# Kernel optimization log

Measured on AMD Instinct MI355X. Metric: run time of the kernel, lower is better.

Reference implementation:

```python
import jax, jax.numpy as jnp
import numpy as np

F = 128; K = 64; SR_CUT = 10.0
NB = 5; NRI = 3; NRA = 2; NRO = 1
N_ATOMS = 10000; N_PAIRS = 320000


def act(x):
    # shifted softplus: softplus(x) - log(2)
    return jax.nn.softplus(x) - jnp.log(2.0).astype(x.dtype)


def residual(x, W1, b1, W2, b2):
    # PhysNet residual: x + dense2(dense1(act(x))) with activation on dense1
    h = act(act(x) @ W1 + b1)
    return x + h @ W2 + b2


def cutoff_fn(D):
    x = D / SR_CUT
    x3 = x * x * x; x4 = x3 * x; x5 = x4 * x
    return jnp.where(x < 1.0, 1.0 - 6.0 * x5 + 15.0 * x4 - 10.0 * x3, 0.0)


def setup_inputs() -> dict:
    key = jax.random.key(0)
    ks = jax.random.split(key, 24)

    def nrm(k, shape, s=0.05):
        return (jax.random.normal(k, shape) * s).astype(jnp.float32)

    inp = {}
    inp["Z"] = jax.random.randint(ks[0], (N_ATOMS,), 1, 95)
    inp["R"] = (jax.random.normal(ks[1], (N_ATOMS, 3)) * 3.0).astype(jnp.float32)
    inp["idx_i"] = jax.random.randint(ks[2], (N_PAIRS,), 0, N_ATOMS)
    inp["idx_j"] = jax.random.randint(ks[3], (N_PAIRS,), 0, N_ATOMS)
    s3 = float(np.sqrt(3.0))
    inp["embeddings"] = jax.random.uniform(ks[4], (95, F), minval=-s3, maxval=s3).astype(jnp.float32)
    inp["rbf_centers"] = jnp.linspace(1.0, float(np.exp(-SR_CUT)), K).astype(jnp.float32)
    width = (0.5 / ((1.0 - float(np.exp(-SR_CUT))) / K)) ** 2
    inp["rbf_widths"] = jnp.full((K,), width, dtype=jnp.float32)
    inp["k2f_W"] = nrm(ks[5], (NB, K, F))
    inp["Wi"] = nrm(ks[6], (NB, F, F)); inp["bi"] = jnp.zeros((NB, F), jnp.float32)
    inp["Wj"] = nrm(ks[7], (NB, F, F)); inp["bj"] = jnp.zeros((NB, F), jnp.float32)
    inp["ri_W1"] = nrm(ks[8], (NB, NRI, F, F)); inp["ri_b1"] = jnp.zeros((NB, NRI, F), jnp.float32)
    inp["ri_W2"] = nrm(ks[9], (NB, NRI, F, F)); inp["ri_b2"] = jnp.zeros((NB, NRI, F), jnp.float32)
    inp["dW"] = nrm(ks[10], (NB, F, F)); inp["db"] = jnp.zeros((NB, F), jnp.float32)
    inp["u"] = jnp.ones((NB, F), jnp.float32)
    inp["ra_W1"] = nrm(ks[11], (NB, NRA, F, F)); inp["ra_b1"] = jnp.zeros((NB, NRA, F), jnp.float32)
    inp["ra_W2"] = nrm(ks[12], (NB, NRA, F, F)); inp["ra_b2"] = jnp.zeros((NB, NRA, F), jnp.float32)
    inp["ro_W1"] = nrm(ks[13], (NB, NRO, F, F)); inp["ro_b1"] = jnp.zeros((NB, NRO, F), jnp.float32)
    inp["ro_W2"] = nrm(ks[14], (NB, NRO, F, F)); inp["ro_b2"] = jnp.zeros((NB, NRO, F), jnp.float32)
    inp["out_W"] = nrm(ks[15], (NB, F, 2))
    inp["Escale"] = jnp.ones((95,), jnp.float32); inp["Eshift"] = jnp.zeros((95,), jnp.float32)
    inp["Qscale"] = jnp.ones((95,), jnp.float32); inp["Qshift"] = jnp.zeros((95,), jnp.float32)
    return inp


def reference(Z, R, idx_i, idx_j, embeddings, rbf_centers, rbf_widths, k2f_W, Wi, bi, Wj, bj,
              ri_W1, ri_b1, ri_W2, ri_b2, dW, db, u, ra_W1, ra_b1, ra_W2, ra_b2,
              ro_W1, ro_b1, ro_W2, ro_b2, out_W, Escale, Eshift, Qscale, Qshift):
    N = R.shape[0]
    # gather-based interatomic distances: gather -> sub -> sumsq -> relu -> sqrt
    dR = R[idx_i] - R[idx_j]                                   # [P,3]
    Dij = jnp.sqrt(jax.nn.relu(jnp.sum(dR * dR, axis=-1)))     # [P]
    # RBF expansion with smooth cutoff
    rbf = cutoff_fn(Dij)[:, None] * jnp.exp(-rbf_widths * (jnp.exp(-Dij)[:, None] - rbf_centers) ** 2)  # [P,K]
    x = embeddings[Z]                                          # [N,F]
    Ea = jnp.zeros((N,), x.dtype)
    Qa = jnp.zeros((N,), x.dtype)
    nhloss = jnp.zeros((), x.dtype)
    last2 = None
    for b in range(NB):
        # --- interaction layer ---
        g = rbf @ k2f_W[b]                                     # [P,F]
        xa = act(x)
        xi = act(xa @ Wi[b] + bi[b])                           # [N,F]
        xj_feat = act(xa @ Wj[b] + bj[b])                      # [N,F]
        msg = g * xj_feat[idx_j]                               # [P,F] gather + modulate
        m = xi + jax.ops.segment_sum(msg, idx_i, num_segments=N)
        for l in range(NRI):
            m = residual(m, ri_W1[b, l], ri_b1[b, l], ri_W2[b, l], ri_b2[b, l])
        m = act(m)
        x = u[b] * x + m @ dW[b] + db[b]
        for l in range(NRA):
            x = residual(x, ra_W1[b, l], ra_b1[b, l], ra_W2[b, l], ra_b2[b, l])
        # --- output block ---
        o = x
        for l in range(NRO):
            o = residual(o, ro_W1[b, l], ro_b1[b, l], ro_W2[b, l], ro_b2[b, l])
        out = act(o) @ out_W[b]                                # [N,2] -> (Ea, Qa)
        Ea = Ea + out[:, 0]
        Qa = Qa + out[:, 1]
        out2 = out * out
        if b > 0:
            nhloss = nhloss + jnp.mean(out2 / (out2 + last2 + 1e-7))
        last2 = out2
    Ea = Escale[Z] * Ea + Eshift[Z]
    Qa = Qscale[Z] * Qa + Qshift[Z]
    return Ea, Qa, Dij, nhloss
```

## Files before the change

kernel.cpp:

```cpp
#include <hip/hip_runtime.h>

typedef __attribute__((ext_vector_type(8))) short bfrag;
typedef __attribute__((ext_vector_type(4))) float ffrag;

__device__ __forceinline__ unsigned short f2b(float f){
  unsigned int u = __float_as_uint(f);
  return (unsigned short)((u + 0x7FFFu + ((u >> 16) & 1u)) >> 16);
}
__device__ __forceinline__ float b2f_lo(unsigned int v){
  return __uint_as_float(v << 16);
}
__device__ __forceinline__ float b2f_hi(unsigned int v){
  return __uint_as_float(v & 0xFFFF0000u);
}
__device__ __forceinline__ int rfl(int v){ return __builtin_amdgcn_readfirstlane(v); }
__device__ __forceinline__ float actf(float v){
  float e = __builtin_amdgcn_exp2f(-fabsf(v)*1.44269504088896341f);
  return fmaxf(v, 0.f) + __builtin_amdgcn_logf(1.f + e)*0.69314718055994531f - 0.69314718055994531f;
}

__global__ __launch_bounds__(256) void k_zero(float* p, int n){
  int i = blockIdx.x*256 + threadIdx.x;
  if (i < n) p[i] = 0.f;
}

__global__ __launch_bounds__(256) void k_dij_count(
    const float* __restrict__ R, const int* __restrict__ idx_i, const int* __restrict__ idx_j,
    float* __restrict__ DijF, float* __restrict__ Dout, int* __restrict__ counts, int P){
  int p = blockIdx.x*256 + threadIdx.x;
  if (p >= P) return;
  int i = idx_i[p], j = idx_j[p];
  float dx = R[i*3+0] - R[j*3+0];
  float dy = R[i*3+1] - R[j*3+1];
  float dz = R[i*3+2] - R[j*3+2];
  float D = sqrtf(fmaxf(dx*dx + dy*dy + dz*dz, 0.f));
  DijF[p] = D;
  Dout[p] = D;
  atomicAdd(&counts[i], 1);
}

__global__ __launch_bounds__(1024) void k_scan(const int* __restrict__ counts,
    int* __restrict__ cursor, int N){
  __shared__ int wsum[16];
  int tid = threadIdx.x;
  int CH = (N + 1023) >> 10;
  int base = tid * CH;
  int s = 0;
  for (int i = 0; i < CH; ++i){
    int idx = base + i;
    s += (idx < N) ? counts[idx] : 0;
  }
  int lane = tid & 63, w = tid >> 6;
  int v = s;
  #pragma unroll
  for (int off = 1; off < 64; off <<= 1){
    int t = __shfl_up(v, off, 64);
    if (lane >= off) v += t;
  }
  if (lane == 63) wsum[w] = v;
  __syncthreads();
  if (tid < 16){
    int t = wsum[tid];
    int vv = t;
    #pragma unroll
    for (int off = 1; off < 16; off <<= 1){
      int u = __shfl_up(vv, off, 64);
      if (tid >= off) vv += u;
    }
    wsum[tid] = vv - t;
  }
  __syncthreads();
  int run = (v - s) + wsum[w];
  for (int i = 0; i < CH; ++i){
    int idx = base + i;
    if (idx < N){ cursor[idx] = run; run += counts[idx]; }
  }
}

__global__ __launch_bounds__(256) void k_scatter(const int* __restrict__ idx_i,
    const int* __restrict__ idx_j, const float* __restrict__ DijF,
    int* __restrict__ cursor, int* __restrict__ i_s, int* __restrict__ j_s,
    float* __restrict__ D_s, int P){
  int p = blockIdx.x*256 + threadIdx.x;
  if (p >= P) return;
  int i = idx_i[p];
  int pos = atomicAdd(&cursor[i], 1);
  i_s[pos] = i;
  j_s[pos] = idx_j[p];
  D_s[pos] = DijF[p];
}

__global__ __launch_bounds__(256) void k_prep2(
    const float* __restrict__ D_s, const float* __restrict__ cent, const float* __restrict__ wid,
    unsigned short* __restrict__ rbf_s,
    const float* __restrict__ riW1, const float* __restrict__ riW2,
    const float* __restrict__ dW,   const float* __restrict__ raW1,
    const float* __restrict__ raW2, const float* __restrict__ roW1,
    const float* __restrict__ roW2, const float* __restrict__ Wi,
    const float* __restrict__ Wj,   const float* __restrict__ k2f,
    const float* __restrict__ outW,
    unsigned short* __restrict__ WBall, unsigned short* __restrict__ k2fP,
    unsigned short* __restrict__ outWB, int P){
  int gid0 = blockIdx.x*256 + threadIdx.x;
  if (gid0 < P*8){
    int t = gid0 >> 3, kg = gid0 & 7;
    float D = D_s[t];
    float xc = D * 0.1f;
    float cut = 0.f;
    if (xc < 1.f){
      float x3 = xc*xc*xc, x4 = x3*xc, x5 = x4*xc;
      cut = 1.f - 6.f*x5 + 15.f*x4 - 10.f*x3;
    }
    float eD = __builtin_amdgcn_exp2f(-D*1.44269504088896341f);
    bfrag o;
    #pragma unroll
    for (int i = 0; i < 8; ++i){
      int k = kg*8 + i;
      float tt = eD - cent[k];
      float v = cut * __builtin_amdgcn_exp2f(-wid[k]*tt*tt*1.44269504088896341f);
      o[i] = (short)f2b(v);
    }
    *(bfrag*)(rbf_s + (size_t)gid0*8) = o;
    return;
  }
  int gid = gid0 - P*8;
  if (gid < 75*2048){
    int i = gid >> 11, r = gid & 2047;
    const float* S;
    int slot;
    if (i < 15)      { S = riW1 + (size_t)i*16384;      slot = (i/3)*15 + 2*(i%3); }
    else if (i < 30) { int j=i-15; S = riW2 + (size_t)j*16384; slot = (j/3)*15 + 2*(j%3) + 1; }
    else if (i < 35) { int j=i-30; S = dW   + (size_t)j*16384; slot = j*15 + 6; }
    else if (i < 45) { int j=i-35; S = raW1 + (size_t)j*16384; slot = (j/2)*15 + 7 + 2*(j%2); }
    else if (i < 55) { int j=i-45; S = raW2 + (size_t)j*16384; slot = (j/2)*15 + 8 + 2*(j%2); }
    else if (i < 60) { int j=i-55; S = roW1 + (size_t)j*16384; slot = j*15 + 11; }
    else if (i < 65) { int j=i-60; S = roW2 + (size_t)j*16384; slot = j*15 + 12; }
    else if (i < 70) { int j=i-65; S = Wi   + (size_t)j*16384; slot = ((j==0)?4:(j-1))*15 + 13; }
    else             { int j=i-70; S = Wj   + (size_t)j*16384; slot = ((j==0)?4:(j-1))*15 + 14; }
    int fr = r >> 6, l = r & 63;
    int T = fr >> 2, k0 = fr & 3;
    int n = T*16 + (l & 15);
    int kbase = k0*32 + (l >> 4)*8;
    unsigned short* D = WBall + ((size_t)slot*2048 + r)*8;
    ushort4 o0, o1;
    o0.x=f2b(S[(kbase+0)*128+n]); o0.y=f2b(S[(kbase+1)*128+n]);
    o0.z=f2b(S[(kbase+2)*128+n]); o0.w=f2b(S[(kbase+3)*128+n]);
    o1.x=f2b(S[(kbase+4)*128+n]); o1.y=f2b(S[(kbase+5)*128+n]);
    o1.z=f2b(S[(kbase+6)*128+n]); o1.w=f2b(S[(kbase+7)*128+n]);
    ((ushort4*)D)[0]=o0; ((ushort4*)D)[1]=o1;
  } else if (gid < 75*2048 + 5120){
    int g = gid - 75*2048;
    int l = g & 63, fr = (g >> 6) & 15, b = g >> 10;
    int tile = fr >> 1, kh = fr & 1;
    const float* src = k2f + (size_t)b*64*128;
    int n = tile*16 + (l & 15);
    int kbase = kh*32 + (l >> 4)*8;
    ushort4 o0, o1;
    o0.x = f2b(src[(kbase+0)*128+n]); o0.y = f2b(src[(kbase+1)*128+n]);
    o0.z = f2b(src[(kbase+2)*128+n]); o0.w = f2b(src[(kbase+3)*128+n]);
    o1.x = f2b(src[(kbase+4)*128+n]); o1.y = f2b(src[(kbase+5)*128+n]);
    o1.z = f2b(src[(kbase+6)*128+n]); o1.w = f2b(src[(kbase+7)*128+n]);
    ushort4* dst = (ushort4*)(k2fP + (size_t)g*8);
    dst[0] = o0; dst[1] = o1;
  } else if (gid < 75*2048 + 5120 + 1280){
    int g = gid - (75*2048 + 5120);
    int b = g >> 8, r = g & 255;
    int l = r & 63;
    int col = l & 15;
    int k0 = r >> 6;
    int kbase = k0*32 + (l >> 4)*8;
    ushort4 o0 = {0,0,0,0}, o1 = {0,0,0,0};
    if (col < 2){
      const float* S = outW + (size_t)b*256;
      o0.x=f2b(S[(kbase+0)*2+col]); o0.y=f2b(S[(kbase+1)*2+col]);
      o0.z=f2b(S[(kbase+2)*2+col]); o0.w=f2b(S[(kbase+3)*2+col]);
      o1.x=f2b(S[(kbase+4)*2+col]); o1.y=f2b(S[(kbase+5)*2+col]);
      o1.z=f2b(S[(kbase+6)*2+col]); o1.w=f2b(S[(kbase+7)*2+col]);
    }
    unsigned short* D = outWB + ((size_t)b*256 + r)*8;
    ((ushort4*)D)[0]=o0; ((ushort4*)D)[1]=o1;
  }
}

__device__ __forceinline__ void mmtile(const unsigned short* tile,
    const unsigned short* __restrict__ WB, int w, int l, ffrag C[4]){
  int m = l & 15, q = l >> 4;
  bfrag A[4];
  #pragma unroll
  for (int k0 = 0; k0 < 4; ++k0)
    A[k0] = *(const bfrag*)(tile + m*136 + k0*32 + q*8);
  #pragma unroll
  for (int tt = 0; tt < 4; ++tt){
    ffrag c = {0.f,0.f,0.f,0.f};
    const bfrag* bp = (const bfrag*)(WB + (((w*4+tt)*4)*64 + l)*8);
    #pragma unroll
    for (int k0 = 0; k0 < 4; ++k0)
      c = __builtin_amdgcn_mfma_f32_16x16x32_bf16(A[k0], bp[k0*64], c, 0, 0, 0);
    C[tt] = c;
  }
}

__global__ __launch_bounds__(128) void k_phase1m(
    const int* __restrict__ Z, const float* __restrict__ emb,
    const unsigned short* __restrict__ WB45,
    const float* __restrict__ bi0, const float* __restrict__ bj0,
    float* __restrict__ x_g, float* __restrict__ m_g, unsigned short* __restrict__ xjb_g, int N){
  __shared__ unsigned short tile[16*136];
  int tid = threadIdx.x, w = tid >> 6, l = tid & 63;
  int m = l & 15, q = l >> 4, rbase = blockIdx.x*16;
  #pragma unroll
  for (int r = 0; r < 4; ++r){
    int row = rbase + q*4 + r;
    int z = Z[row];
    #pragma unroll
    for (int tt = 0; tt < 4; ++tt){
      int c = (w*4+tt)*16 + m;
      float v = emb[(size_t)z*128 + c];
      x_g[(size_t)row*128 + c] = v;
      tile[(q*4+r)*136 + c] = f2b(actf(v));
    }
  }
  __syncthreads();
  ffrag C[4];
  mmtile(tile, WB45 + 13*16384, w, l, C);
  #pragma unroll
  for (int tt = 0; tt < 4; ++tt){
    int c = (w*4+tt)*16 + m;
    float bb = bi0[c];
    #pragma unroll
    for (int r = 0; r < 4; ++r)
      m_g[(size_t)(rbase + q*4 + r)*128 + c] = actf(C[tt][r] + bb);
  }
  mmtile(tile, WB45 + 14*16384, w, l, C);
  #pragma unroll
  for (int tt = 0; tt < 4; ++tt){
    int c = (w*4+tt)*16 + m;
    float bb = bj0[c];
    #pragma unroll
    for (int r = 0; r < 4; ++r)
      xjb_g[(size_t)(rbase + q*4 + r)*128 + c] = f2b(actf(C[tt][r] + bb));
  }
}

__global__ __launch_bounds__(256, 4) void k_pairmsg2(
    const unsigned short* __restrict__ rbf_s, const unsigned short* __restrict__ k2fP,
    const int* __restrict__ i_s, const int* __restrict__ j_s,
    const unsigned short* __restrict__ xj, float* __restrict__ m_g, int P){
  __shared__ float G[4][16*130];
  int tid = threadIdx.x, w = tid >> 6, l = tid & 63;
  float* Gw = &G[w][0];
  bfrag B[16];
  #pragma unroll
  for (int t = 0; t < 16; ++t)
    B[t] = *(const bfrag*)(k2fP + (size_t)(t*64 + l)*8);
  int wstart = (blockIdx.x*4 + w)*64;
  if (wstart >= P) return;
  int row16 = l & 15, quad = l >> 4;
  float a0 = 0.f, a1 = 0.f;
  int iCur = -1;
  #pragma unroll 1
  for (int bi2 = 0; bi2 < 4; ++bi2){
    int bt = wstart + bi2*16;
    bfrag A0 = *(const bfrag*)(rbf_s + (size_t)(bt + row16)*64 + quad*8);
    bfrag A1 = *(const bfrag*)(rbf_s + (size_t)(bt + row16)*64 + 32 + quad*8);
    int ip[16], jp[16];
    #pragma unroll
    for (int g = 0; g < 4; ++g){
      int4 it = *(const int4*)(i_s + bt + g*4);
      int4 jt = *(const int4*)(j_s + bt + g*4);
      ip[g*4+0]=rfl(it.x); ip[g*4+1]=rfl(it.y); ip[g*4+2]=rfl(it.z); ip[g*4+3]=rfl(it.w);
      jp[g*4+0]=rfl(jt.x); jp[g*4+1]=rfl(jt.y); jp[g*4+2]=rfl(jt.z); jp[g*4+3]=rfl(jt.w);
    }
    unsigned int xv[16];
    #pragma unroll
    for (int k = 0; k < 16; ++k)
      xv[k] = *(const unsigned int*)(xj + (size_t)jp[k]*128 + 2*l);
    #pragma unroll
    for (int t = 0; t < 8; ++t){
      ffrag C = {0.f,0.f,0.f,0.f};
      C = __builtin_amdgcn_mfma_f32_16x16x32_bf16(A0, B[t*2],   C, 0, 0, 0);
      C = __builtin_amdgcn_mfma_f32_16x16x32_bf16(A1, B[t*2+1], C, 0, 0, 0);
      #pragma unroll
      for (int r = 0; r < 4; ++r)
        Gw[(quad*4+r)*130 + t*16 + row16] = C[r];
    }
    #pragma unroll
    for (int k = 0; k < 16; ++k){
      int i = ip[k];
      if (i != iCur){
        if (iCur >= 0){
          unsafeAtomicAdd(&m_g[(size_t)iCur*128 + 2*l],     a0);
          unsafeAtomicAdd(&m_g[(size_t)iCur*128 + 2*l + 1], a1);
        }
        iCur = i; a0 = 0.f; a1 = 0.f;
      }
      float g0 = Gw[k*130 + 2*l], g1 = Gw[k*130 + 2*l + 1];
      a0 = fmaf(g0, b2f_lo(xv[k]), a0);
      a1 = fmaf(g1, b2f_hi(xv[k]), a1);
    }
  }
  if (iCur >= 0){
    unsafeAtomicAdd(&m_g[(size_t)iCur*128 + 2*l],     a0);
    unsafeAtomicAdd(&m_g[(size_t)iCur*128 + 2*l + 1], a1);
  }
}

template<int HASNEXT, int NH>
__global__ __launch_bounds__(512) void k_phase2m(
    float* __restrict__ m_g, float* __restrict__ x_g, unsigned short* __restrict__ xjb_g,
    const unsigned short* __restrict__ WBb,
    const float* __restrict__ rib1, const float* __restrict__ rib2,
    const float* __restrict__ db, const float* __restrict__ u,
    const float* __restrict__ rab1, const float* __restrict__ rab2,
    const float* __restrict__ rob1, const float* __restrict__ rob2,
    const float* __restrict__ biN, const float* __restrict__ bjN,
    const unsigned short* __restrict__ outWBb,
    float* __restrict__ Ea, float* __restrict__ Qa,
    float* __restrict__ last2, float* __restrict__ nh, int N){
  __shared__ unsigned short tiles[2][2][16*136];
  __shared__ float biasS[16*128];
  int tid = threadIdx.x, w = tid >> 6, l = tid & 63;
  int m = l & 15, q = l >> 4, rbase = blockIdx.x*32;
  int c = w*16 + m;
  ffrag mC[2], xC[2], C[2];
  float xrow[2][4];
  int cur = 0;
  const int nst = HASNEXT ? 15 : 13;
  const int slotSeq[15] = {0,1,2,3,4,5,6,7,8,9,10,
                           HASNEXT?13:11, HASNEXT?14:12, 11, 12};
  bfrag Bb[2][4];
  #pragma unroll
  for (int k0 = 0; k0 < 4; ++k0)
    Bb[0][k0] = *(const bfrag*)(WBb + (size_t)slotSeq[0]*16384 + (size_t)((w*4+k0)*64 + l)*8);

  if (tid < 128){
    biasS[0*128+tid]  = rib1[tid];
    biasS[1*128+tid]  = rib1[128+tid];
    biasS[2*128+tid]  = rib1[256+tid];
    biasS[3*128+tid]  = rib2[tid];
    biasS[4*128+tid]  = rib2[128+tid];
    biasS[5*128+tid]  = rib2[256+tid];
    biasS[6*128+tid]  = db[tid];
    biasS[7*128+tid]  = u[tid];
    biasS[8*128+tid]  = rab1[tid];
    biasS[9*128+tid]  = rab1[128+tid];
    biasS[10*128+tid] = rab2[tid];
    biasS[11*128+tid] = rab2[128+tid];
    biasS[12*128+tid] = rob1[tid];
    biasS[13*128+tid] = rob2[tid];
    biasS[14*128+tid] = biN[tid];
    biasS[15*128+tid] = bjN[tid];
  }
  #pragma unroll
  for (int h = 0; h < 2; ++h){
    #pragma unroll
    for (int r = 0; r < 4; ++r){
      int row = rbase + h*16 + q*4 + r;
      int rs = row < N ? row : N-1;
      xrow[h][r] = x_g[(size_t)rs*128 + c];
      float v = m_g[(size_t)rs*128 + c];
      mC[h][r] = v;
      tiles[h][0][(q*4+r)*136 + c] = f2b(actf(v));
    }
  }
  #pragma unroll 2
  for (int s = 0; s < nst; ++s){
    __syncthreads();
    if (s+1 < nst){
      #pragma unroll
      for (int k0 = 0; k0 < 4; ++k0)
        Bb[(s+1)&1][k0] = *(const bfrag*)(WBb + (size_t)slotSeq[s+1]*16384 + (size_t)((w*4+k0)*64 + l)*8);
    }
    #pragma unroll
    for (int h = 0; h < 2; ++h){
      const unsigned short* tp = &tiles[h][cur][0];
      ffrag cc = {0.f,0.f,0.f,0.f};
      #pragma unroll
      for (int k0 = 0; k0 < 4; ++k0){
        bfrag A = *(const bfrag*)(tp + m*136 + k0*32 + q*8);
        cc = __builtin_amdgcn_mfma_f32_16x16x32_bf16(A, Bb[s&1][k0], cc, 0, 0, 0);
      }
      C[h] = cc;
    }
    if (HASNEXT && s == 11){
      float bb = biasS[14*128 + c];
      #pragma unroll
      for (int h = 0; h < 2; ++h)
        #pragma unroll
        for (int r = 0; r < 4; ++r){
          int row = rbase + h*16 + q*4 + r;
          if (row < N) m_g[(size_t)row*128 + c] = actf(C[h][r] + bb);
        }
    } else if (HASNEXT && s == 12){
      float bb = biasS[15*128 + c];
      #pragma unroll
      for (int h = 0; h < 2; ++h)
        #pragma unroll
        for (int r = 0; r < 4; ++r){
          int row = rbase + h*16 + q*4 + r;
          if (row < N) xjb_g[(size_t)row*128 + c] = f2b(actf(C[h][r] + bb));
        }
    } else if (s == 6){
      float uu = biasS[7*128 + c], bb = biasS[6*128 + c];
      #pragma unroll
      for (int h = 0; h < 2; ++h)
        #pragma unroll
        for (int r = 0; r < 4; ++r){
          float nv = uu*xrow[h][r] + C[h][r] + bb;
          xC[h][r] = nv;
          tiles[h][1-cur][(q*4+r)*136 + c] = f2b(actf(nv));
        }
      cur ^= 1;
    } else if (s == 1 || s == 3 || s == 5){
      float bb = biasS[(3 + (s>>1))*128 + c];
      #pragma unroll
      for (int h = 0; h < 2; ++h)
        #pragma unroll
        for (int r = 0; r < 4; ++r){
          float nv = mC[h][r] + C[h][r] + bb;
          mC[h][r] = nv;
          tiles[h][1-cur][(q*4+r)*136 + c] = f2b(actf(nv));
        }
      cur ^= 1;
    } else if (s == 8 || s == 10){
      float bb = biasS[(10 + ((s-8)>>1))*128 + c];
      #pragma unroll
      for (int h = 0; h < 2; ++h)
        #pragma unroll
        for (int r = 0; r < 4; ++r){
          float nv = xC[h][r] + C[h][r] + bb;
          xC[h][r] = nv;
          tiles[h][1-cur][(q*4+r)*136 + c] = f2b(actf(nv));
          if (HASNEXT && s == 10){
            int row = rbase + h*16 + q*4 + r;
            if (row < N) x_g[(size_t)row*128 + c] = nv;
          }
        }
      cur ^= 1;
    } else if ((HASNEXT && s == 14) || (!HASNEXT && s == 12)){
      float bb = biasS[13*128 + c];
      #pragma unroll
      for (int h = 0; h < 2; ++h)
        #pragma unroll
        for (int r = 0; r < 4; ++r){
          float ov = xC[h][r] + C[h][r] + bb;
          tiles[h][1-cur][(q*4+r)*136 + c] = f2b(actf(ov));
        }
      cur ^= 1;
    } else {
      int bidx = (s==0)?0:(s==2)?1:(s==4)?2:(s==7)?8:(s==9)?9:12;
      float bb = biasS[bidx*128 + c];
      #pragma unroll
      for (int h = 0; h < 2; ++h)
        #pragma unroll
        for (int r = 0; r < 4; ++r)
          tiles[h][1-cur][(q*4+r)*136 + c] = f2b(actf(C[h][r] + bb));
      cur ^= 1;
    }
  }
  __syncthreads();
  if (w < 2){
    const unsigned short* tp = &tiles[w][cur][0];
    bfrag A[4];
    #pragma unroll
    for (int k0 = 0; k0 < 4; ++k0)
      A[k0] = *(const bfrag*)(tp + m*136 + k0*32 + q*8);
    ffrag Ch = {0.f,0.f,0.f,0.f};
    #pragma unroll
    for (int k0 = 0; k0 < 4; ++k0){
      bfrag B = *(const bfrag*)(outWBb + (size_t)(k0*64 + l)*8);
      Ch = __builtin_amdgcn_mfma_f32_16x16x32_bf16(A[k0], B, Ch, 0, 0, 0);
    }
    int col = m;
    if (col < 2){
      float tpa = 0.f;
      #pragma unroll
      for (int r = 0; r < 4; ++r){
        int row = rbase + w*16 + q*4 + r;
        if (row < N){
          float val = Ch[r];
          if (NH){
            if (col == 0) Ea[row] += val; else Qa[row] += val;
          } else {
            if (col == 0) Ea[row]  = val; else Qa[row]  = val;
          }
          float sq = val*val;
          if (NH){
            float lastv = last2[row*2 + col];
            tpa += sq/(sq + lastv + 1e-7f);
          }
          last2[row*2 + col] = sq;
        }
      }
      if (NH) unsafeAtomicAdd(nh, tpa);
    }
  }
}

__global__ __launch_bounds__(256) void k_final(
    const int* __restrict__ Z, const float* __restrict__ Ea, const float* __restrict__ Qa,
    const float* __restrict__ Es, const float* __restrict__ Eh,
    const float* __restrict__ Qs, const float* __restrict__ Qh,
    const float* __restrict__ nh, float* __restrict__ out, int N, int P){
  int n = blockIdx.x*256 + threadIdx.x;
  if (n < N){
    int z = Z[n];
    out[n]   = Es[z]*Ea[n] + Eh[z];
    out[N+n] = Qs[z]*Qa[n] + Qh[z];
  }
  if (blockIdx.x == 0 && threadIdx.x == 0)
    out[(size_t)2*N + P] = nh[0] / (2.f * (float)N);
}

extern "C" void kernel_launch(void* const* d_in, const int* in_sizes, int n_in,
                              void* d_out, int out_size, void* d_ws, size_t ws_size,
                              hipStream_t stream){
  const int N = in_sizes[0];
  const int P = in_sizes[2];
  const int F = 128;

  const int* Z      = (const int*)d_in[0];
  const float* R    = (const float*)d_in[1];
  const int* idx_i  = (const int*)d_in[2];
  const int* idx_j  = (const int*)d_in[3];
  const float* emb  = (const float*)d_in[4];
  const float* cent = (const float*)d_in[5];
  const float* wid  = (const float*)d_in[6];
  const float* k2f  = (const float*)d_in[7];
  const float* Wi   = (const float*)d_in[8];  const float* bi   = (const float*)d_in[9];
  const float* Wj   = (const float*)d_in[10]; const float* bj   = (const float*)d_in[11];
  const float* riW1 = (const float*)d_in[12]; const float* rib1 = (const float*)d_in[13];
  const float* riW2 = (const float*)d_in[14]; const float* rib2 = (const float*)d_in[15];
  const float* dWp  = (const float*)d_in[16]; const float* dbp  = (const float*)d_in[17];
  const float* u    = (const float*)d_in[18];
  const float* raW1 = (const float*)d_in[19]; const float* rab1 = (const float*)d_in[20];
  const float* raW2 = (const float*)d_in[21]; const float* rab2 = (const float*)d_in[22];
  const float* roW1 = (const float*)d_in[23]; const float* rob1 = (const float*)d_in[24];
  const float* roW2 = (const float*)d_in[25]; const float* rob2 = (const float*)d_in[26];
  const float* outW = (const float*)d_in[27];
  const float* Es   = (const float*)d_in[28]; const float* Eh   = (const float*)d_in[29];
  const float* Qs   = (const float*)d_in[30]; const float* Qh   = (const float*)d_in[31];

  char* ws = (char*)d_ws;
  size_t off = 0;
  float* DijF  = (float*)(ws + off); off += (size_t)P*4;
  float* D_s   = (float*)(ws + off); off += (size_t)P*4;
  int*   i_s   = (int*)  (ws + off); off += (size_t)P*4;
  int*   j_s   = (int*)  (ws + off); off += (size_t)P*4;
  unsigned short* rbf_s = (unsigned short*)(ws + off); off += (size_t)P*64*2;
  unsigned short* k2fP  = (unsigned short*)(ws + off); off += (size_t)5*16*64*8*2;
  unsigned short* WBall = (unsigned short*)(ws + off); off += (size_t)75*16384*2;
  unsigned short* outWB = (unsigned short*)(ws + off); off += (size_t)5*2048*2;
  float* x     = (float*)(ws + off); off += (size_t)N*F*4;
  unsigned short* xjb = (unsigned short*)(ws + off); off += (size_t)N*F*2;
  float* m     = (float*)(ws + off); off += (size_t)N*F*4;
  float* last2 = (float*)(ws + off); off += (size_t)N*2*4;
  float* Ea    = (float*)(ws + off); off += (size_t)N*4;
  float* Qa    = (float*)(ws + off); off += (size_t)N*4;
  float* nh    = (float*)(ws + off); off += 256;
  int*   counts= (int*)  (ws + off); off += (size_t)N*4;
  int*   cursor= (int*)  (ws + off); off += (size_t)N*4;

  float* outF = (float*)d_out;
  float* Dout = outF + (size_t)2*N;

  const int nzero = N + 64;
  k_zero<<<dim3((nzero+255)/256), dim3(256), 0, stream>>>(nh, nzero);
  k_dij_count<<<dim3((P+255)/256), dim3(256), 0, stream>>>(R, idx_i, idx_j, DijF, Dout, counts, P);
  k_scan<<<dim3(1), dim3(1024), 0, stream>>>(counts, cursor, N);
  k_scatter<<<dim3((P+255)/256), dim3(256), 0, stream>>>(idx_i, idx_j, DijF, cursor, i_s, j_s, D_s, P);
  const int prep2n = P*8 + 75*2048 + 5120 + 1280;
  k_prep2<<<dim3((prep2n+255)/256), dim3(256), 0, stream>>>(
      D_s, cent, wid, rbf_s,
      riW1, riW2, dWp, raW1, raW2, roW1, roW2, Wi, Wj, k2f, outW,
      WBall, k2fP, outWB, P);

  const int G16 = (N + 15)/16;
  k_phase1m<<<dim3(G16), dim3(128), 0, stream>>>(Z, emb, WBall + (size_t)4*15*16384,
                                                 bi, bj, x, m, xjb, N);

  const int pmg = (P + 255)/256;
  const int G32 = (N + 31)/32;
  for (int b = 0; b < 5; ++b){
    k_pairmsg2<<<dim3(pmg), dim3(256), 0, stream>>>(rbf_s, k2fP + (size_t)b*16*64*8,
                                                    i_s, j_s, xjb, m, P);
    const unsigned short* WBb = WBall + (size_t)b*15*16384;
    const float* a_rib1 = rib1 + (size_t)b*3*F;
    const float* a_rib2 = rib2 + (size_t)b*3*F;
    const float* a_db   = dbp  + (size_t)b*F;
    const float* a_u    = u    + (size_t)b*F;
    const float* a_rab1 = rab1 + (size_t)b*2*F;
    const float* a_rab2 = rab2 + (size_t)b*2*F;
    const float* a_rob1 = rob1 + (size_t)b*F;
    const float* a_rob2 = rob2 + (size_t)b*F;
    int bn = (b < 4) ? (b+1) : 0;
    const float* a_biN = bi + (size_t)bn*F;
    const float* a_bjN = bj + (size_t)bn*F;
    const unsigned short* oWB = outWB + (size_t)b*2048;
    if (b == 0){
      k_phase2m<1,0><<<dim3(G32), dim3(512), 0, stream>>>(m, x, xjb, WBb,
        a_rib1, a_rib2, a_db, a_u, a_rab1, a_rab2, a_rob1, a_rob2,
        a_biN, a_bjN, oWB, Ea, Qa, last2, nh, N);
    } else if (b < 4){
      k_phase2m<1,1><<<dim3(G32), dim3(512), 0, stream>>>(m, x, xjb, WBb,
        a_rib1, a_rib2, a_db, a_u, a_rab1, a_rab2, a_rob1, a_rob2,
        a_biN, a_bjN, oWB, Ea, Qa, last2, nh, N);
    } else {
      k_phase2m<0,1><<<dim3(G32), dim3(512), 0, stream>>>(m, x, xjb, WBb,
        a_rib1, a_rib2, a_db, a_u, a_rab1, a_rab2, a_rob1, a_rob2,
        a_biN, a_bjN, oWB, Ea, Qa, last2, nh, N);
    }
  }
  k_final<<<dim3((N+255)/256), dim3(256), 0, stream>>>(Z, Ea, Qa, Es, Eh, Qs, Qh, nh, outF, N, P);
}
```

Before: 440.4 us.

## Fuse per-block pair-message and atom-update kernels into one cooperative persistent kernel

Replaces the ten per-interaction-block launches (pair message kernel plus atom-update kernel) with a single cooperative persistent kernel. It loops over the five blocks and separates the phases with grid-wide syncs. The atom phase now uses 256-thread blocks over 16-row tiles instead of 512 threads over 32 rows, reusing the shared memory of the pair phase. This removes launch gaps and tail effects between kernels, at the cost of grid-sync overhead, grid size capped by occupancy, and less per-tile weight reuse. Bias tables are reloaded on every tile, and runtime branches replace the earlier template specialisation.

```diff
diff --git a/kernel.cpp b/kernel.cpp
--- a/kernel.cpp
+++ b/kernel.cpp
@@ -1,4 +1,7 @@
 #include <hip/hip_runtime.h>
+#include <hip/hip_cooperative_groups.h>
+
+namespace cg = cooperative_groups;
 
 typedef __attribute__((ext_vector_type(8))) short bfrag;
 typedef __attribute__((ext_vector_type(4))) float ffrag;
@@ -199,6 +202,30 @@
     C[tt] = c;
   }
 }
+__device__ __forceinline__ void loadB8(const unsigned short* __restrict__ WB,
+    int w, int l, bfrag* B){
+  #pragma unroll
+  for (int tt = 0; tt < 2; ++tt)
+    #pragma unroll
+    for (int k0 = 0; k0 < 4; ++k0)
+      B[tt*4+k0] = *(const bfrag*)(WB + ((size_t)((((w*2+tt)*4)+k0)*64 + l))*8);
+}
+__device__ __forceinline__ void mmB(const unsigned short* tile, const bfrag* B,
+    int l, ffrag C[2]){
+  int m = l & 15, q = l >> 4;
+  bfrag A[4];
+  #pragma unroll
+  for (int k0 = 0; k0 < 4; ++k0)
+    A[k0] = *(const bfrag*)(tile + m*136 + k0*32 + q*8);
+  #pragma unroll
+  for (int tt = 0; tt < 2; ++tt){
+    ffrag c = {0.f,0.f,0.f,0.f};
+    #pragma unroll
+    for (int k0 = 0; k0 < 4; ++k0)
+      c = __builtin_amdgcn_mfma_f32_16x16x32_bf16(A[k0], B[tt*4+k0], c, 0, 0, 0);
+    C[tt] = c;
+  }
+}
 
 __global__ __launch_bounds__(128) void k_phase1m(
     const int* __restrict__ Z, const float* __restrict__ emb,
@@ -242,258 +269,280 @@
   }
 }
 
-__global__ __launch_bounds__(256, 4) void k_pairmsg2(
-    const unsigned short* __restrict__ rbf_s, const unsigned short* __restrict__ k2fP,
-    const int* __restrict__ i_s, const int* __restrict__ j_s,
-    const unsigned short* __restrict__ xj, float* __restrict__ m_g, int P){
-  __shared__ float G[4][16*130];
+struct BParams {
+  const unsigned short* rbf_s;
+  const unsigned short* k2fP;
+  const int* i_s; const int* j_s;
+  unsigned short* xjb;
+  float* m_g; float* x_g;
+  const unsigned short* WBall;
+  const float* rib1; const float* rib2; const float* dbp; const float* uu;
+  const float* rab1; const float* rab2; const float* rob1; const float* rob2;
+  const float* bi; const float* bj;
+  const unsigned short* outWB;
+  float* Ea; float* Qa; float* last2; float* nh;
+  int N; int P;
+};
+
+__global__ __launch_bounds__(256) void k_bloop(BParams p){
+  cg::grid_group gg = cg::this_grid();
+  __shared__ float Gs[4][16*130];
+  unsigned short* tilesS = (unsigned short*)&Gs[0][0];
+  float* biasS = (float*)((char*)&Gs[0][0] + 8704);
   int tid = threadIdx.x, w = tid >> 6, l = tid & 63;
-  float* Gw = &G[w][0];
-  bfrag B[16];
-  #pragma unroll
-  for (int t = 0; t < 16; ++t)
-    B[t] = *(const bfrag*)(k2fP + (size_t)(t*64 + l)*8);
-  int wstart = (blockIdx.x*4 + w)*64;
-  if (wstart >= P) return;
-  int row16 = l & 15, quad = l >> 4;
-  float a0 = 0.f, a1 = 0.f;
-  int iCur = -1;
-  #pragma unroll 1
-  for (int bi2 = 0; bi2 < 4; ++bi2){
-    int bt = wstart + bi2*16;
-    bfrag A0 = *(const bfrag*)(rbf_s + (size_t)(bt + row16)*64 + quad*8);
-    bfrag A1 = *(const bfrag*)(rbf_s + (size_t)(bt + row16)*64 + 32 + quad*8);
-    int ip[16], jp[16];
-    #pragma unroll
-    for (int g = 0; g < 4; ++g){
-      int4 it = *(const int4*)(i_s + bt + g*4);
-      int4 jt = *(const int4*)(j_s + bt + g*4);
-      ip[g*4+0]=rfl(it.x); ip[g*4+1]=rfl(it.y); ip[g*4+2]=rfl(it.z); ip[g*4+3]=rfl(it.w);
-      jp[g*4+0]=rfl(jt.x); jp[g*4+1]=rfl(jt.y); jp[g*4+2]=rfl(jt.z); jp[g*4+3]=rfl(jt.w);
-    }
-    unsigned int xv[16];
-    #pragma unroll
-    for (int k = 0; k < 16; ++k)
-      xv[k] = *(const unsigned int*)(xj + (size_t)jp[k]*128 + 2*l);
-    #pragma unroll
-    for (int t = 0; t < 8; ++t){
-      ffrag C = {0.f,0.f,0.f,0.f};
-      C = __builtin_amdgcn_mfma_f32_16x16x32_bf16(A0, B[t*2],   C, 0, 0, 0);
-      C = __builtin_amdgcn_mfma_f32_16x16x32_bf16(A1, B[t*2+1], C, 0, 0, 0);
+  int m16 = l & 15, q = l >> 4;
+  const int F = 128;
+  int nT = (p.N + 15) >> 4;
+
+  for (int b = 0; b < 5; ++b){
+    int hasnext = (b < 4) ? 1 : 0;
+    int nh_on   = (b > 0) ? 1 : 0;
+    {
+      const unsigned short* k2fPb = p.k2fP + (size_t)b*16*64*8;
+      bfrag B[16];
       #pragma unroll
-      for (int r = 0; r < 4; ++r)
-        Gw[(quad*4+r)*130 + t*16 + row16] = C[r];
-    }
-    #pragma unroll
-    for (int k = 0; k < 16; ++k){
-      int i = ip[k];
-      if (i != iCur){
-        if (iCur >= 0){
-          unsafeAtomicAdd(&m_g[(size_t)iCur*128 + 2*l],     a0);
-          unsafeAtomicAdd(&m_g[(size_t)iCur*128 + 2*l + 1], a1);
-        }
-        iCur = i; a0 = 0.f; a1 = 0.f;
-      }
-      float g0 = Gw[k*130 + 2*l], g1 = Gw[k*130 + 2*l + 1];
-      a0 = fmaf(g0, b2f_lo(xv[k]), a0);
-      a1 = fmaf(g1, b2f_hi(xv[k]), a1);
-    }
-  }
-  if (iCur >= 0){
-    unsafeAtomicAdd(&m_g[(size_t)iCur*128 + 2*l],     a0);
-    unsafeAtomicAdd(&m_g[(size_t)iCur*128 + 2*l + 1], a1);
-  }
-}
-
-template<int HASNEXT, int NH>
-__global__ __launch_bounds__(512) void k_phase2m(
-    float* __restrict__ m_g, float* __restrict__ x_g, unsigned short* __restrict__ xjb_g,
-    const unsigned short* __restrict__ WBb,
-    const float* __restrict__ rib1, const float* __restrict__ rib2,
-    const float* __restrict__ db, const float* __restrict__ u,
-    const float* __restrict__ rab1, const float* __restrict__ rab2,
-    const float* __restrict__ rob1, const float* __restrict__ rob2,
-    const float* __restrict__ biN, const float* __restrict__ bjN,
-    const unsigned short* __restrict__ outWBb,
-    float* __restrict__ Ea, float* __restrict__ Qa,
-    float* __restrict__ last2, float* __restrict__ nh, int N){
-  __shared__ unsigned short tiles[2][2][16*136];
-  __shared__ float biasS[16*128];
-  int tid = threadIdx.x, w = tid >> 6, l = tid & 63;
-  int m = l & 15, q = l >> 4, rbase = blockIdx.x*32;
-  int c = w*16 + m;
-  ffrag mC[2], xC[2], C[2];
-  float xrow[2][4];
-  int cur = 0;
-  const int nst = HASNEXT ? 15 : 13;
-  const int slotSeq[15] = {0,1,2,3,4,5,6,7,8,9,10,
-                           HASNEXT?13:11, HASNEXT?14:12, 11, 12};
-  bfrag Bb[2][4];
-  #pragma unroll
-  for (int k0 = 0; k0 < 4; ++k0)
-    Bb[0][k0] = *(const bfrag*)(WBb + (size_t)slotSeq[0]*16384 + (size_t)((w*4+k0)*64 + l)*8);
-
-  if (tid < 128){
-    biasS[0*128+tid]  = rib1[tid];
-    biasS[1*128+tid]  = rib1[128+tid];
-    biasS[2*128+tid]  = rib1[256+tid];
-    biasS[3*128+tid]  = rib2[tid];
-    biasS[4*128+tid]  = rib2[128+tid];
-    biasS[5*128+tid]  = rib2[256+tid];
-    biasS[6*128+tid]  = db[tid];
-    biasS[7*128+tid]  = u[tid];
-    biasS[8*128+tid]  = rab1[tid];
-    biasS[9*128+tid]  = rab1[128+tid];
-    biasS[10*128+tid] = rab2[tid];
-    biasS[11*128+tid] = rab2[128+tid];
-    biasS[12*128+tid] = rob1[tid];
-    biasS[13*128+tid] = rob2[tid];
-    biasS[14*128+tid] = biN[tid];
-    biasS[15*128+tid] = bjN[tid];
-  }
-  #pragma unroll
-  for (int h = 0; h < 2; ++h){
-    #pragma unroll
-    for (int r = 0; r < 4; ++r){
-      int row = rbase + h*16 + q*4 + r;
-      int rs = row < N ? row : N-1;
-      xrow[h][r] = x_g[(size_t)rs*128 + c];
-      float v = m_g[(size_t)rs*128 + c];
-      mC[h][r] = v;
-      tiles[h][0][(q*4+r)*136 + c] = f2b(actf(v));
-    }
-  }
-  #pragma unroll 2
-  for (int s = 0; s < nst; ++s){
-    __syncthreads();
-    if (s+1 < nst){
-      #pragma unroll
-      for (int k0 = 0; k0 < 4; ++k0)
-        Bb[(s+1)&1][k0] = *(const bfrag*)(WBb + (size_t)slotSeq[s+1]*16384 + (size_t)((w*4+k0)*64 + l)*8);
-    }
-    #pragma unroll
-    for (int h = 0; h < 2; ++h){
-      const unsigned short* tp = &tiles[h][cur][0];
-      ffrag cc = {0.f,0.f,0.f,0.f};
-      #pragma unroll
-      for (int k0 = 0; k0 < 4; ++k0){
-        bfrag A = *(const bfrag*)(tp + m*136 + k0*32 + q*8);
-        cc = __builtin_amdgcn_mfma_f32_16x16x32_bf16(A, Bb[s&1][k0], cc, 0, 0, 0);
-      }
-      C[h] = cc;
-    }
-    if (HASNEXT && s == 11){
-      float bb = biasS[14*128 + c];
-      #pragma unroll
-      for (int h = 0; h < 2; ++h)
-        #pragma unroll
-        for (int r = 0; r < 4; ++r){
-          int row = rbase + h*16 + q*4 + r;
-          if (row < N) m_g[(size_t)row*128 + c] = actf(C[h][r] + bb);
-        }
-    } else if (HASNEXT && s == 12){
-      float bb = biasS[15*128 + c];
-      #pragma unroll
-      for (int h = 0; h < 2; ++h)
-        #pragma unroll
-        for (int r = 0; r < 4; ++r){
-          int row = rbase + h*16 + q*4 + r;
-          if (row < N) xjb_g[(size_t)row*128 + c] = f2b(actf(C[h][r] + bb));
-        }
-    } else if (s == 6){
-      float uu = biasS[7*128 + c], bb = biasS[6*128 + c];
-      #pragma unroll
-      for (int h = 0; h < 2; ++h)
-        #pragma unroll
-        for (int r = 0; r < 4; ++r){
-          float nv = uu*xrow[h][r] + C[h][r] + bb;
-          xC[h][r] = nv;
-          tiles[h][1-cur][(q*4+r)*136 + c] = f2b(actf(nv));
-        }
-      cur ^= 1;
-    } else if (s == 1 || s == 3 || s == 5){
-      float bb = biasS[(3 + (s>>1))*128 + c];
-      #pragma unroll
-      for (int h = 0; h < 2; ++h)
-        #pragma unroll
-        for (int r = 0; r < 4; ++r){
-          float nv = mC[h][r] + C[h][r] + bb;
-          mC[h][r] = nv;
-          tiles[h][1-cur][(q*4+r)*136 + c] = f2b(actf(nv));
-        }
-      cur ^= 1;
-    } else if (s == 8 || s == 10){
-      float bb = biasS[(10 + ((s-8)>>1))*128 + c];
-      #pragma unroll
-      for (int h = 0; h < 2; ++h)
-        #pragma unroll
-        for (int r = 0; r < 4; ++r){
-          float nv = xC[h][r] + C[h][r] + bb;
-          xC[h][r] = nv;
-          tiles[h][1-cur][(q*4+r)*136 + c] = f2b(actf(nv));
-          if (HASNEXT && s == 10){
-            int row = rbase + h*16 + q*4 + r;
-            if (row < N) x_g[(size_t)row*128 + c] = nv;
+      for (int t = 0; t < 16; ++t)
+        B[t] = *(const bfrag*)(k2fPb + (size_t)(t*64 + l)*8);
+      float* Gw = &Gs[w][0];
+      int nseg = (p.P + 63) >> 6;
+      int nwv = gridDim.x * 4;
+      for (int seg = blockIdx.x*4 + w; seg < nseg; seg += nwv){
+        int wstart = seg << 6;
+        float a0 = 0.f, a1 = 0.f;
+        int iCur = -1;
+        #pragma unroll 1
+        for (int bi2 = 0; bi2 < 4; ++bi2){
+          int bt = wstart + bi2*16;
+          bfrag A0 = *(const bfrag*)(p.rbf_s + (size_t)(bt + m16)*64 + q*8);
+          bfrag A1 = *(const bfrag*)(p.rbf_s + (size_t)(bt + m16)*64 + 32 + q*8);
+          int ip[16], jp[16];
+          #pragma unroll
+          for (int g = 0; g < 4; ++g){
+            int4 it = *(const int4*)(p.i_s + bt + g*4);
+            int4 jt = *(const int4*)(p.j_s + bt + g*4);
+            ip[g*4+0]=rfl(it.x); ip[g*4+1]=rfl(it.y); ip[g*4+2]=rfl(it.z); ip[g*4+3]=rfl(it.w);
+            jp[g*4+0]=rfl(jt.x); jp[g*4+1]=rfl(jt.y); jp[g*4+2]=rfl(jt.z); jp[g*4+3]=rfl(jt.w);
+          }
+          unsigned int xv[16];
+          #pragma unroll
+          for (int k = 0; k < 16; ++k)
+            xv[k] = *(const unsigned int*)(p.xjb + (size_t)jp[k]*128 + 2*l);
+          #pragma unroll
+          for (int t = 0; t < 8; ++t){
+            ffrag C = {0.f,0.f,0.f,0.f};
+            C = __builtin_amdgcn_mfma_f32_16x16x32_bf16(A0, B[t*2],   C, 0, 0, 0);
+            C = __builtin_amdgcn_mfma_f32_16x16x32_bf16(A1, B[t*2+1], C, 0, 0, 0);
+            #pragma unroll
+            for (int r = 0; r < 4; ++r)
+              Gw[(q*4+r)*130 + t*16 + m16] = C[r];
+          }
+          #pragma unroll
+          for (int k = 0; k < 16; ++k){
+            int i = ip[k];
+            if (i != iCur){
+              if (iCur >= 0){
+                unsafeAtomicAdd(&p.m_g[(size_t)iCur*128 + 2*l],     a0);
+                unsafeAtomicAdd(&p.m_g[(size_t)iCur*128 + 2*l + 1], a1);
+              }
+              iCur = i; a0 = 0.f; a1 = 0.f;
+            }
+            float g0 = Gw[k*130 + 2*l], g1 = Gw[k*130 + 2*l + 1];
+            a0 = fmaf(g0, b2f_lo(xv[k]), a0);
+            a1 = fmaf(g1, b2f_hi(xv[k]), a1);
           }
         }
-      cur ^= 1;
-    } else if ((HASNEXT && s == 14) || (!HASNEXT && s == 12)){
-      float bb = biasS[13*128 + c];
-      #pragma unroll
-      for (int h = 0; h < 2; ++h)
-        #pragma unroll
-        for (int r = 0; r < 4; ++r){
-          float ov = xC[h][r] + C[h][r] + bb;
-          tiles[h][1-cur][(q*4+r)*136 + c] = f2b(actf(ov));
-        }
-      cur ^= 1;
-    } else {
-      int bidx = (s==0)?0:(s==2)?1:(s==4)?2:(s==7)?8:(s==9)?9:12;
-      float bb = biasS[bidx*128 + c];
-      #pragma unroll
-      for (int h = 0; h < 2; ++h)
-        #pragma unroll
-        for (int r = 0; r < 4; ++r)
-          tiles[h][1-cur][(q*4+r)*136 + c] = f2b(actf(C[h][r] + bb));
-      cur ^= 1;
-    }
-  }
-  __syncthreads();
-  if (w < 2){
-    const unsigned short* tp = &tiles[w][cur][0];
-    bfrag A[4];
-    #pragma unroll
-    for (int k0 = 0; k0 < 4; ++k0)
-      A[k0] = *(const bfrag*)(tp + m*136 + k0*32 + q*8);
-    ffrag Ch = {0.f,0.f,0.f,0.f};
-    #pragma unroll
-    for (int k0 = 0; k0 < 4; ++k0){
-      bfrag B = *(const bfrag*)(outWBb + (size_t)(k0*64 + l)*8);
-      Ch = __builtin_amdgcn_mfma_f32_16x16x32_bf16(A[k0], B, Ch, 0, 0, 0);
-    }
-    int col = m;
-    if (col < 2){
-      float tpa = 0.f;
-      #pragma unroll
-      for (int r = 0; r < 4; ++r){
-        int row = rbase + w*16 + q*4 + r;
-        if (row < N){
-          float val = Ch[r];
-          if (NH){
-            if (col == 0) Ea[row] += val; else Qa[row] += val;
-          } else {
-            if (col == 0) Ea[row]  = val; else Qa[row]  = val;
-          }
-          float sq = val*val;
-          if (NH){
-            float lastv = last2[row*2 + col];
-            tpa += sq/(sq + lastv + 1e-7f);
-          }
-          last2[row*2 + col] = sq;
+        if (iCur >= 0){
+          unsafeAtomicAdd(&p.m_g[(size_t)iCur*128 + 2*l],     a0);
+          unsafeAtomicAdd(&p.m_g[(size_t)iCur*128 + 2*l + 1], a1);
         }
       }
-      if (NH) unsafeAtomicAdd(nh, tpa);
     }
+    gg.sync();
+    {
+      const unsigned short* WBb = p.WBall + (size_t)b*15*16384;
+      const unsigned short* oWB = p.outWB + (size_t)b*2048;
+      const float* rib1 = p.rib1 + (size_t)b*3*F;
+      const float* rib2 = p.rib2 + (size_t)b*3*F;
+      const float* dbb  = p.dbp  + (size_t)b*F;
+      const float* ub   = p.uu   + (size_t)b*F;
+      const float* rab1 = p.rab1 + (size_t)b*2*F;
+      const float* rab2 = p.rab2 + (size_t)b*2*F;
+      const float* rob1 = p.rob1 + (size_t)b*F;
+      const float* rob2 = p.rob2 + (size_t)b*F;
+      int bn = hasnext ? (b+1) : 0;
+      const float* biN = p.bi + (size_t)bn*F;
+      const float* bjN = p.bj + (size_t)bn*F;
+      int nst = hasnext ? 15 : 13;
+      auto slot_of = [&](int s)->int{
+        int t = s;
+        if (s >= 11 && hasnext) t = (s < 13) ? s + 2 : s - 2;
+        return t;
+      };
+      for (int tile0 = blockIdx.x; tile0 < nT; tile0 += gridDim.x){
+        int rbase = tile0*16;
+        if (tid < 128){
+          biasS[0*128+tid]  = rib1[tid];
+          biasS[1*128+tid]  = rib1[128+tid];
+          biasS[2*128+tid]  = rib1[256+tid];
+          biasS[3*128+tid]  = rib2[tid];
+          biasS[4*128+tid]  = rib2[128+tid];
+          biasS[5*128+tid]  = rib2[256+tid];
+          biasS[6*128+tid]  = dbb[tid];
+          biasS[7*128+tid]  = ub[tid];
+          biasS[8*128+tid]  = rab1[tid];
+          biasS[9*128+tid]  = rab1[128+tid];
+          biasS[10*128+tid] = rab2[tid];
+          biasS[11*128+tid] = rab2[128+tid];
+          biasS[12*128+tid] = rob1[tid];
+          biasS[13*128+tid] = rob2[tid];
+          biasS[14*128+tid] = biN[tid];
+          biasS[15*128+tid] = bjN[tid];
+        }
+        ffrag mC[2], xC[2], C[2];
+        float xrow[2][4];
+        int cur = 0;
+        bfrag Bb2[2][8];
+        loadB8(WBb + (size_t)slot_of(0)*16384, w, l, Bb2[0]);
+        #pragma unroll
+        for (int tt = 0; tt < 2; ++tt){
+          int c = (w*2+tt)*16 + m16;
+          #pragma unroll
+          for (int r = 0; r < 4; ++r){
+            int row = rbase + q*4 + r;
+            xrow[tt][r] = p.x_g[(size_t)row*128 + c];
+            float v = p.m_g[(size_t)row*128 + c];
+            mC[tt][r] = v;
+            tilesS[0*2176 + (q*4+r)*136 + c] = f2b(actf(v));
+          }
+        }
+        #pragma unroll 1
+        for (int s = 0; s < nst; ++s){
+          __syncthreads();
+          if (s+1 < nst) loadB8(WBb + (size_t)slot_of(s+1)*16384, w, l, Bb2[(s+1)&1]);
+          mmB(tilesS + cur*2176, Bb2[s&1], l, C);
+          if (hasnext && s == 11){
+            #pragma unroll
+            for (int tt = 0; tt < 2; ++tt){
+              int c = (w*2+tt)*16 + m16;
+              float bb = biasS[14*128 + c];
+              #pragma unroll
+              for (int r = 0; r < 4; ++r)
+                p.m_g[(size_t)(rbase + q*4 + r)*128 + c] = actf(C[tt][r] + bb);
+            }
+          } else if (hasnext && s == 12){
+            #pragma unroll
+            for (int tt = 0; tt < 2; ++tt){
+              int c = (w*2+tt)*16 + m16;
+              float bb = biasS[15*128 + c];
+              #pragma unroll
+              for (int r = 0; r < 4; ++r)
+                p.xjb[(size_t)(rbase + q*4 + r)*128 + c] = f2b(actf(C[tt][r] + bb));
+            }
+          } else if (s == 6){
+            #pragma unroll
+            for (int tt = 0; tt < 2; ++tt){
+              int c = (w*2+tt)*16 + m16;
+              float uuv = biasS[7*128 + c], bb = biasS[6*128 + c];
+              #pragma unroll
+              for (int r = 0; r < 4; ++r){
+                float nv = uuv*xrow[tt][r] + C[tt][r] + bb;
+                xC[tt][r] = nv;
+                tilesS[(1-cur)*2176 + (q*4+r)*136 + c] = f2b(actf(nv));
+              }
+            }
+            cur ^= 1;
+          } else if (s == 1 || s == 3 || s == 5){
+            #pragma unroll
+            for (int tt = 0; tt < 2; ++tt){
+              int c = (w*2+tt)*16 + m16;
+              float bb = biasS[(3 + (s>>1))*128 + c];
+              #pragma unroll
+              for (int r = 0; r < 4; ++r){
+                float nv = mC[tt][r] + C[tt][r] + bb;
+                mC[tt][r] = nv;
+                tilesS[(1-cur)*2176 + (q*4+r)*136 + c] = f2b(actf(nv));
+              }
+            }
+            cur ^= 1;
+          } else if (s == 8 || s == 10){
+            #pragma unroll
+            for (int tt = 0; tt < 2; ++tt){
+              int c = (w*2+tt)*16 + m16;
+              float bb = biasS[(10 + ((s-8)>>1))*128 + c];
+              #pragma unroll
+              for (int r = 0; r < 4; ++r){
+                float nv = xC[tt][r] + C[tt][r] + bb;
+                xC[tt][r] = nv;
+                tilesS[(1-cur)*2176 + (q*4+r)*136 + c] = f2b(actf(nv));
+                if (hasnext && s == 10)
+                  p.x_g[(size_t)(rbase + q*4 + r)*128 + c] = nv;
+              }
+            }
+            cur ^= 1;
+          } else if ((hasnext && s == 14) || (!hasnext && s == 12)){
+            #pragma unroll
+            for (int tt = 0; tt < 2; ++tt){
+              int c = (w*2+tt)*16 + m16;
+              float bb = biasS[13*128 + c];
+              #pragma unroll
+              for (int r = 0; r < 4; ++r){
+                float ov = xC[tt][r] + C[tt][r] + bb;
+                tilesS[(1-cur)*2176 + (q*4+r)*136 + c] = f2b(actf(ov));
+              }
+            }
+            cur ^= 1;
+          } else {
+            int bidx = (s==0)?0:(s==2)?1:(s==4)?2:(s==7)?8:(s==9)?9:12;
+            #pragma unroll
+            for (int tt = 0; tt < 2; ++tt){
+              int c = (w*2+tt)*16 + m16;
+              float bb = biasS[bidx*128 + c];
+              #pragma unroll
+              for (int r = 0; r < 4; ++r)
+                tilesS[(1-cur)*2176 + (q*4+r)*136 + c] = f2b(actf(C[tt][r] + bb));
+            }
+            cur ^= 1;
+          }
+        }
+        __syncthreads();
+        if (w == 0){
+          const unsigned short* tp = tilesS + cur*2176;
+          bfrag A[4];
+          #pragma unroll
+          for (int k0 = 0; k0 < 4; ++k0)
+            A[k0] = *(const bfrag*)(tp + m16*136 + k0*32 + q*8);
+          ffrag Ch = {0.f,0.f,0.f,0.f};
+          #pragma unroll
+          for (int k0 = 0; k0 < 4; ++k0){
+            bfrag B = *(const bfrag*)(oWB + (size_t)(k0*64 + l)*8);
+            Ch = __builtin_amdgcn_mfma_f32_16x16x32_bf16(A[k0], B, Ch, 0, 0, 0);
+          }
+          int col = m16;
+          if (col < 2){
+            float tpa = 0.f;
+            #pragma unroll
+            for (int r = 0; r < 4; ++r){
+              int row = rbase + q*4 + r;
+              float val = Ch[r];
+              if (nh_on){
+                if (col == 0) p.Ea[row] += val; else p.Qa[row] += val;
+              } else {
+                if (col == 0) p.Ea[row]  = val; else p.Qa[row]  = val;
+              }
+              float sq = val*val;
+              if (nh_on){
+                float lastv = p.last2[row*2 + col];
+                tpa += sq/(sq + lastv + 1e-7f);
+              }
+              p.last2[row*2 + col] = sq;
+            }
+            if (nh_on) unsafeAtomicAdd(p.nh, tpa);
+          }
+        }
+        __syncthreads();
+      }
+    }
+    gg.sync();
   }
 }
 
@@ -579,37 +628,32 @@
   k_phase1m<<<dim3(G16), dim3(128), 0, stream>>>(Z, emb, WBall + (size_t)4*15*16384,
                                                  bi, bj, x, m, xjb, N);
 
-  const int pmg = (P + 255)/256;
-  const int G32 = (N + 31)/32;
-  for (int b = 0; b < 5; ++b){
-    k_pairmsg2<<<dim3(pmg), dim3(256), 0, stream>>>(rbf_s, k2fP + (size_t)b*16*64*8,
-                                                    i_s, j_s, xjb, m, P);
-    const unsigned short* WBb = WBall + (size_t)b*15*16384;
-    const float* a_rib1 = rib1 + (size_t)b*3*F;
-    const float* a_rib2 = rib2 + (size_t)b*3*F;
-    const float* a_db   = dbp  + (size_t)b*F;
-    const float* a_u    = u    + (size_t)b*F;
-    const float* a_rab1 = rab1 + (size_t)b*2*F;
-    const float* a_rab2 = rab2 + (size_t)b*2*F;
-    const float* a_rob1 = rob1 + (size_t)b*F;
-    const float* a_rob2 = rob2 + (size_t)b*F;
-    int bn = (b < 4) ? (b+1) : 0;
-    const float* a_biN = bi + (size_t)bn*F;
-    const float* a_bjN = bj + (size_t)bn*F;
-    const unsigned short* oWB = outWB + (size_t)b*2048;
-    if (b == 0){
-      k_phase2m<1,0><<<dim3(G32), dim3(512), 0, stream>>>(m, x, xjb, WBb,
-        a_rib1, a_rib2, a_db, a_u, a_rab1, a_rab2, a_rob1, a_rob2,
-        a_biN, a_bjN, oWB, Ea, Qa, last2, nh, N);
-    } else if (b < 4){
-      k_phase2m<1,1><<<dim3(G32), dim3(512), 0, stream>>>(m, x, xjb, WBb,
-        a_rib1, a_rib2, a_db, a_u, a_rab1, a_rab2, a_rob1, a_rob2,
-        a_biN, a_bjN, oWB, Ea, Qa, last2, nh, N);
-    } else {
-      k_phase2m<0,1><<<dim3(G32), dim3(512), 0, stream>>>(m, x, xjb, WBb,
-        a_rib1, a_rib2, a_db, a_u, a_rab1, a_rab2, a_rob1, a_rob2,
-        a_biN, a_bjN, oWB, Ea, Qa, last2, nh, N);
-    }
-  }
+  static int capBlocks = -1;
+  if (capBlocks < 0){
+    hipDeviceProp_t prop;
+    hipGetDeviceProperties(&prop, 0);
+    int nb = 0;
+    hipOccupancyMaxActiveBlocksPerMultiprocessor(&nb, k_bloop, 256, 0);
+    if (nb < 1) nb = 1;
+    capBlocks = nb * prop.multiProcessorCount;
+  }
+  int grid = capBlocks;
+  int pairBlocks = (P + 255)/256;
+  if (grid > pairBlocks) grid = pairBlocks;
+  if (grid < 1) grid = 1;
+
+  BParams bp;
+  bp.rbf_s = rbf_s; bp.k2fP = k2fP; bp.i_s = i_s; bp.j_s = j_s;
+  bp.xjb = xjb; bp.m_g = m; bp.x_g = x;
+  bp.WBall = WBall;
+  bp.rib1 = rib1; bp.rib2 = rib2; bp.dbp = dbp; bp.uu = u;
+  bp.rab1 = rab1; bp.rab2 = rab2; bp.rob1 = rob1; bp.rob2 = rob2;
+  bp.bi = bi; bp.bj = bj;
+  bp.outWB = outWB;
+  bp.Ea = Ea; bp.Qa = Qa; bp.last2 = last2; bp.nh = nh;
+  bp.N = N; bp.P = P;
+  void* kargs[] = { (void*)&bp };
+  hipLaunchCooperativeKernel((void*)k_bloop, dim3(grid), dim3(256), kargs, 0, stream);
+
   k_final<<<dim3((N+255)/256), dim3(256), 0, stream>>>(Z, Ea, Qa, Es, Eh, Qs, Qh, nh, outF, N, P);
 }
```

Result: slower. 1.350 ms (+206.5%).
